# Kernel optimization log

Measured on AMD Instinct MI355X. Metric: run time of the kernel, lower is better.

## Reference

```python
import jax, jax.numpy as jnp
import numpy as np

D_STATE = 16
D_CONV = 4


def _diag_perm(H, W):
    perm = []
    for off in range(-(H - 1), W):
        for i in range(H):
            j = i + off
            if 0 <= j < W:
                perm.append(i * W + j)
    perm = np.asarray(perm, dtype=np.int32)
    inv = np.argsort(perm).astype(np.int32)
    return perm, inv


def _mamba_block(x, W_in, conv_w, W_xproj, W_dt, b_dt, A_log, W_outm):
    # x: [B, L, E]; shared-weight SimplifiedMambaBlock, expand=1 -> d_inner = E
    Bsz, L, E = x.shape
    d_inner = W_in.shape[1] // 2
    d_state = W_xproj.shape[1] // 2
    xz = x @ W_in                              # [B, L, 2*d_inner]
    xi, z = xz[..., :d_inner], xz[..., d_inner:]
    # causal depthwise conv1d (padding=d_conv-1, trimmed to L)
    xc = jax.lax.conv_general_dilated(
        xi.transpose(0, 2, 1), conv_w, window_strides=(1,),
        padding=[(conv_w.shape[-1] - 1, 0)], feature_group_count=d_inner,
        dimension_numbers=('NCH', 'OIH', 'NCH'))
    xc = jax.nn.silu(xc.transpose(0, 2, 1))    # [B, L, d_inner]
    dtbc = xc @ W_xproj                        # [B, L, 2*d_state]
    dt = jax.nn.softplus(dtbc[..., :d_state] @ W_dt + b_dt)  # [B, L, d_inner]
    Bc = dtbc[..., d_state:]                   # [B, L, d_state]
    A = -jnp.exp(A_log)                        # [d_inner, d_state]

    def step(h, inp):
        dt_t, B_t, x_t = inp                   # [B,d_inner], [B,d_state], [B,d_inner]
        h = h * jnp.exp(A[None] * dt_t[:, :, None]) + B_t[:, None, :] * x_t[:, :, None]
        return h, h.sum(-1)

    h0 = jnp.zeros((Bsz, d_inner, d_state), x.dtype)
    _, y = jax.lax.scan(step, h0, (dt.transpose(1, 0, 2), Bc.transpose(1, 0, 2), xc.transpose(1, 0, 2)))
    y = y.transpose(1, 0, 2)                   # [B, L, d_inner]
    return (y * jax.nn.silu(z)) @ W_outm


def setup_inputs() -> dict:
    key = jax.random.key(0)
    ks = jax.random.split(key, 16)
    B, H, W, E = 8, 32, 32, 1024
    d_inner, d_state = E, D_STATE
    s = lambda n: 1.0 / np.sqrt(n)
    A = np.tile(np.arange(1, d_state + 1, dtype=np.float32), (d_inner, 1))
    return {
        'vision_features': jax.random.normal(ks[0], (B, H * W, E), jnp.float32),
        'W_input': jax.random.normal(ks[1], (E, E), jnp.float32) * s(E),
        'W_in': jax.random.normal(ks[2], (E, 2 * d_inner), jnp.float32) * s(E),
        'conv_w': jax.random.normal(ks[3], (d_inner, 1, D_CONV), jnp.float32) * s(D_CONV),
        'W_xproj': jax.random.normal(ks[4], (d_inner, 2 * d_state), jnp.float32) * s(d_inner),
        'W_dt': jax.random.normal(ks[5], (d_state, d_inner), jnp.float32) * s(d_state),
        'b_dt': jax.random.normal(ks[6], (d_inner,), jnp.float32) * 0.01,
        'A_log': jnp.asarray(np.log(A)),
        'W_outm': jax.random.normal(ks[7], (d_inner, E), jnp.float32) * s(d_inner),
        'dir_w': jnp.full((4,), 0.25, jnp.float32),
        'ln_g': jnp.ones((E,), jnp.float32),
        'ln_b': jnp.zeros((E,), jnp.float32),
        'W_outproj': jax.random.normal(ks[8], (E, E), jnp.float32) * s(E),
        'Wg1': jax.random.normal(ks[9], (E, E // 4), jnp.float32) * s(E),
        'Wg2': jax.random.normal(ks[10], (E // 4, 1), jnp.float32) * s(E // 4),
        'height': H,
        'width': W,
    }


def reference(vision_features, W_input, W_in, conv_w, W_xproj, W_dt, b_dt, A_log,
              W_outm, dir_w, ln_g, ln_b, W_outproj, Wg1, Wg2, height, width):
    B, N, E = vision_features.shape
    H, Wd = int(height), int(width)
    mamba = lambda t: _mamba_block(t, W_in, conv_w, W_xproj, W_dt, b_dt, A_log, W_outm)
    x = vision_features @ W_input              # [B, N, E]
    x2d = x.reshape(B, H, Wd, E)
    # direction 1: row-major
    out1 = mamba(x)
    # direction 2: flipped both spatial dims
    xf = jnp.flip(x2d, (1, 2)).reshape(B, N, E)
    out2 = jnp.flip(mamba(xf).reshape(B, H, Wd, E), (1, 2)).reshape(B, N, E)
    # direction 3: column-major (transpose)
    xt = x2d.transpose(0, 2, 1, 3).reshape(B, N, E)
    out3 = mamba(xt).reshape(B, Wd, H, E).transpose(0, 2, 1, 3).reshape(B, N, E)
    # direction 4: anti-diagonal scan
    perm, inv = _diag_perm(H, Wd)
    out4 = mamba(x[:, perm])[:, inv]
    fused = dir_w[0] * out1 + dir_w[1] * out2 + dir_w[2] * out3 + dir_w[3] * out4
    mu = fused.mean(-1, keepdims=True)
    var = ((fused - mu) ** 2).mean(-1, keepdims=True)
    fused = (fused - mu) * jax.lax.rsqrt(var + 1e-5) * ln_g + ln_b
    enhanced = fused @ W_outproj
    g = jax.nn.sigmoid(jax.nn.silu(vision_features.mean(1, keepdims=True) @ Wg1) @ Wg2)  # [B,1,1]
    return vision_features + g * enhanced
```

## Files before the change

### kernel.cpp

```cpp
#include <hip/hip_runtime.h>

typedef unsigned short u16;
typedef unsigned int u32;
typedef short v8s __attribute__((ext_vector_type(8)));
typedef float v4f __attribute__((ext_vector_type(4)));
typedef float v2f __attribute__((ext_vector_type(2)));

#define B_SZ 8
#define HH 32
#define WW 32
#define NN 1024
#define M1 (B_SZ * NN)
#define M4 (4 * M1)
#define NCHUNK 32
#define CLEN 32
#define CTB 8

__device__ __forceinline__ float bf2f(u16 u) {
    u32 x = ((u32)u) << 16;
    return __builtin_bit_cast(float, x);
}
__device__ __forceinline__ u16 f2bf(float f) {
    u32 x = __builtin_bit_cast(u32, f);
    x = x + 0x7fffu + ((x >> 16) & 1u);
    return (u16)(x >> 16);
}
__device__ __forceinline__ float sigmoidf_(float x) { return 1.f / (1.f + __expf(-x)); }
__device__ __forceinline__ float ldf(const void* p, size_t i, int fin) {
    return fin ? ((const float*)p)[i] : bf2f(((const u16*)p)[i]);
}
__device__ __forceinline__ u16 ldbf(const void* p, size_t i, int fin) {
    return fin ? f2bf(((const float*)p)[i]) : ((const u16*)p)[i];
}
__device__ __forceinline__ void gload_lds16(const u16* g, u16* l) {
    __builtin_amdgcn_global_load_lds(
        (const __attribute__((address_space(1))) unsigned int*)g,
        (__attribute__((address_space(3))) unsigned int*)l, 16, 0, 0);
}
__device__ __forceinline__ int dirmap(int d, int t, const int* __restrict__ perm3) {
    if (d == 0) return t;
    if (d == 1) return (NN - 1) - t;
    if (d == 2) return (t & (HH - 1)) * WW + (t >> 5);
    return perm3[t];
}

__global__ void detect_dtype(const u16* __restrict__ raw, int* __restrict__ flags) {
    if (threadIdx.x == 0 && blockIdx.x == 0) {
        int ok = 0;
        for (int i = 0; i < 512; i++) {
            int e = (raw[i] >> 7) & 0xFF;
            ok += (e >= 100 && e <= 140) ? 1 : 0;
        }
        flags[0] = (ok < 460) ? 1 : 0;
    }
}

__global__ __launch_bounds__(256) void convert_bf(const void* __restrict__ src,
                                                  u16* __restrict__ dst,
                                                  const int* __restrict__ flags, int n) {
    int fin = flags[0];
    int i = blockIdx.x * 256 + threadIdx.x;
    if (i < n) dst[i] = ldbf(src, (size_t)i, fin);
}

__global__ __launch_bounds__(256) void zero_f32(float* __restrict__ p, int n) {
    int i = blockIdx.x * 256 + threadIdx.x;
    if (i < n) p[i] = 0.f;
}

__global__ void diag_perm_init(int* __restrict__ perm, int* __restrict__ inv) {
    int t = blockIdx.x * blockDim.x + threadIdx.x;
    if (t >= NN) return;
    int i = t / WW, j = t % WW;
    int off = j - i;
    int start = 0;
    for (int o = -(HH - 1); o < off; ++o) {
        int lo = (0 > -o) ? 0 : -o;
        int hi = (HH - 1 < WW - 1 - o) ? (HH - 1) : (WW - 1 - o);
        start += (hi - lo + 1);
    }
    int lo0 = (0 > -off) ? 0 : -off;
    int r = start + (i - lo0);
    perm[r] = t;
    inv[t] = r;
}

__global__ __launch_bounds__(256) void transpose_pad(const void* __restrict__ src,
                                                     u16* __restrict__ dst,
                                                     int K, int Nsrc,
                                                     const int* __restrict__ flags) {
    int fin = flags[0];
    __shared__ u16 tile[32][33];
    int k0 = blockIdx.x * 32, n0 = blockIdx.y * 32;
    int tx = threadIdx.x & 31, ty = threadIdx.x >> 5;
#pragma unroll
    for (int i = 0; i < 4; i++) {
        int k = k0 + ty + i * 8, n = n0 + tx;
        tile[ty + i * 8][tx] = (n < Nsrc) ? ldbf(src, (size_t)k * Nsrc + n, fin) : (u16)0;
    }
    __syncthreads();
#pragma unroll
    for (int i = 0; i < 4; i++) {
        int n = n0 + ty + i * 8, k = k0 + tx;
        dst[(size_t)n * K + k] = tile[tx][ty + i * 8];
    }
}

template <int EM>
__global__ __launch_bounds__(256) void gemm128(const u16* __restrict__ A,
                                               const u16* __restrict__ Bt,
                                               void* __restrict__ out0,
                                               void* __restrict__ out1,
                                               int M, int N, int K,
                                               const int* __restrict__ flags,
                                               const void* __restrict__ aux0,
                                               const float* __restrict__ aux1) {
    int fin = flags[0];
    __shared__ __align__(16) u16 As[128][32];
    __shared__ __align__(16) u16 Bs[128][32];
    int tid = threadIdx.x;
    int wave = tid >> 6, lane = tid & 63, quad = lane >> 4, l16 = lane & 15;
    int wm = wave >> 1, wn = wave & 1;
    int m0 = blockIdx.x * 128, n0 = blockIdx.y * 128;
    int r = tid >> 2, p = tid & 3;
    int sA = ((p ^ ((r >> 1) & 3))) * 8;

    const u16* rA0 = A + (size_t)(m0 + r) * K;
    const u16* rA1 = A + (size_t)(m0 + 64 + r) * K;
    const u16* rB0 = Bt + (size_t)(n0 + r) * K;
    const u16* rB1 = Bt + (size_t)(n0 + 64 + r) * K;

    v4f acc[4][4];
#pragma unroll
    for (int i = 0; i < 4; i++)
#pragma unroll
        for (int j = 0; j < 4; j++) acc[i][j] = (v4f){0.f, 0.f, 0.f, 0.f};

    int swf = ((l16 >> 1) & 3);
    for (int k0 = 0; k0 < K; k0 += 32) {
        gload_lds16(rA0 + k0 + sA, &As[r][p * 8]);
        gload_lds16(rA1 + k0 + sA, &As[64 + r][p * 8]);
        gload_lds16(rB0 + k0 + sA, &Bs[r][p * 8]);
        gload_lds16(rB1 + k0 + sA, &Bs[64 + r][p * 8]);
        __syncthreads();
        v8s af[4], bf[4];
#pragma unroll
        for (int i = 0; i < 4; i++)
            af[i] = *(const v8s*)&As[wm * 64 + i * 16 + l16][(quad ^ swf) * 8];
#pragma unroll
        for (int j = 0; j < 4; j++)
            bf[j] = *(const v8s*)&Bs[wn * 64 + j * 16 + l16][(quad ^ swf) * 8];
#pragma unroll
        for (int i = 0; i < 4; i++)
#pragma unroll
            for (int j = 0; j < 4; j++)
                acc[i][j] = __builtin_amdgcn_mfma_f32_16x16x32_bf16(af[i], bf[j],
                                                                    acc[i][j], 0, 0, 0);
        __syncthreads();
    }

#pragma unroll
    for (int i = 0; i < 4; i++) {
#pragma unroll
        for (int j = 0; j < 4; j++) {
#pragma unroll
            for (int rr = 0; rr < 4; rr++) {
                int row = m0 + wm * 64 + i * 16 + quad * 4 + rr;
                int col = n0 + wn * 64 + j * 16 + l16;
                float v = acc[i][j][rr];
                size_t oi = (size_t)row * N + col;
                if (EM == 0) {
                    ((u16*)out0)[oi] = f2bf(v);
                } else if (EM == 1) {
                    if (col < 1024) ((u16*)out0)[(size_t)row * 1024 + col] = f2bf(v);
                    else ((u16*)out1)[(size_t)row * 1024 + (col - 1024)] = f2bf(v);
                } else {
                    float g = aux1[row >> 10];
                    float res = ldf(aux0, oi, fin) + g * v;
                    if (fin) ((float*)out0)[oi] = res;
                    else ((u16*)out0)[oi] = f2bf(res);
                }
            }
        }
    }
}

__global__ __launch_bounds__(256) void gemm_dtbc_ks(const u16* __restrict__ A,
                                                    const u16* __restrict__ Bt,
                                                    float* __restrict__ out0,
                                                    int M, int N, int K) {
    __shared__ u16 As[64][32];
    __shared__ u16 Bs[64][32];
    int tid = threadIdx.x;
    int wave = tid >> 6, lane = tid & 63, quad = lane >> 4, l16 = lane & 15;
    int m0 = blockIdx.x * 64;
    int kbase = blockIdx.y * 128;
    int lr = tid >> 2, p = tid & 3;
    int sA = ((p ^ ((lr >> 1) & 3))) * 8;
    const u16* arow = A + (size_t)(m0 + lr) * K + kbase;
    const u16* brow = Bt + (size_t)lr * K + kbase;
    v4f acc[4];
#pragma unroll
    for (int j = 0; j < 4; j++) acc[j] = (v4f){0.f, 0.f, 0.f, 0.f};
    int swf = ((l16 >> 1) & 3);
    for (int k0 = 0; k0 < 128; k0 += 32) {
        uint4 av = *(const uint4*)(arow + k0 + sA);
        uint4 bv = *(const uint4*)(brow + k0 + sA);
        *(uint4*)&As[lr][p * 8] = av;
        *(uint4*)&Bs[lr][p * 8] = bv;
        __syncthreads();
        v8s af = *(const v8s*)&As[wave * 16 + l16][(quad ^ swf) * 8];
#pragma unroll
        for (int j = 0; j < 4; j++) {
            v8s bf = *(const v8s*)&Bs[j * 16 + l16][(quad ^ swf) * 8];
            acc[j] = __builtin_amdgcn_mfma_f32_16x16x32_bf16(af, bf, acc[j], 0, 0, 0);
        }
        __syncthreads();
    }
#pragma unroll
    for (int j = 0; j < 4; j++)
#pragma unroll
        for (int rr = 0; rr < 4; rr++) {
            int row = m0 + wave * 16 + quad * 4 + rr;
            int col = j * 16 + l16;
            atomicAdd(&out0[(size_t)row * N + col], acc[j][rr]);
        }
}

__global__ __launch_bounds__(256) void conv_tile(const u16* __restrict__ xi,
                                                 const void* __restrict__ cw,
                                                 u16* __restrict__ xc4,
                                                 const int* __restrict__ flags,
                                                 const int* __restrict__ perm3) {
    int fin = flags[0];
    int gblk = blockIdx.x;
    int d = gblk >> 10, blk = gblk & 1023;
    int b = blk >> 7, tc = blk & 127;
    int t0 = tc * CTB;
    __shared__ u16 rows[CTB + 3][1024];
    __shared__ int sp[CTB + 3];
    if (threadIdx.x < CTB + 3) {
        int tt = t0 - 3 + (int)threadIdx.x;
        sp[threadIdx.x] = (tt >= 0) ? dirmap(d, tt, perm3) : -1;
    }
    __syncthreads();
    for (int i = threadIdx.x; i < (CTB + 3) * 128; i += 256) {
        int r = i >> 7, off = (i & 127) * 8;
        int src = sp[r];
        uint4 v = make_uint4(0, 0, 0, 0);
        if (src >= 0)
            v = *(const uint4*)(xi + ((size_t)(b * 1024 + src)) * 1024 + off);
        *(uint4*)&rows[r][off] = v;
    }
    int e0 = threadIdx.x * 4;
    float w[4][4];
#pragma unroll
    for (int ee = 0; ee < 4; ee++)
#pragma unroll
        for (int k = 0; k < 4; k++)
            w[ee][k] = ldf(cw, (size_t)(e0 + ee) * 4 + k, fin);
    __syncthreads();
    u16* outp = xc4 + (size_t)d * M1 * 1024;
#pragma unroll
    for (int t = 0; t < CTB; t++) {
        float a[4] = {0.f, 0.f, 0.f, 0.f};
#pragma unroll
        for (int k = 0; k < 4; k++) {
            uint2 v = *(const uint2*)&rows[t + k][e0];
            const u16* vs = (const u16*)&v;
#pragma unroll
            for (int ee = 0; ee < 4; ee++)
                a[ee] += w[ee][k] * bf2f(vs[ee]);
        }
        u16 o[4];
#pragma unroll
        for (int ee = 0; ee < 4; ee++) o[ee] = f2bf(a[ee] * sigmoidf_(a[ee]));
        *(uint2*)(outp + ((size_t)(b * 1024 + t0 + t)) * 1024 + e0) = *(const uint2*)o;
    }
}

#define SCAN_TLOOP(FASTV)                                                      \
    for (int t = 0; t < CLEN; t++) {                                           \
        float xn = 0.f, zn = 0.f;                                              \
        if (t + 1 < CLEN) {                                                    \
            xn = bf2f(xcyz[ix + 1024]);                                        \
            if (PASS == 3) zn = bf2f(zb[zbase + (size_t)s_perm[t + 1] * 1024]);\
        }                                                                      \
        v2f xpv = {bd, 0.f};                                                   \
        _Pragma("unroll")                                                      \
        for (int p = 0; p < 8; p++)                                            \
            xpv += (*(const v2f*)&sdt[t][2 * p]) * wdt2[p];                    \
        float xp = xpv.x + xpv.y;                                              \
        float ex = __expf(xp);                                                 \
        float dtv = (xp > 15.f) ? xp : __logf(1.f + ex);                       \
        v2f acc2 = {0.f, 0.f};                                                 \
        if (FASTV) {                                                           \
            float E = __expf(-dtv);                                            \
            v2f Ev; Ev.x = E; Ev.y = E * E;                                    \
            v2f Estep; Estep.x = Ev.y; Estep.y = Ev.y;                         \
            _Pragma("unroll")                                                  \
            for (int p = 0; p < 8; p++) {                                      \
                v2f bc = *(const v2f*)&sdt[t][16 + 2 * p];                     \
                h2[p] = h2[p] * Ev + bc * xv;                                  \
                acc2 += h2[p];                                                 \
                Ev *= Estep;                                                   \
            }                                                                  \
        } else {                                                               \
            _Pragma("unroll")                                                  \
            for (int p = 0; p < 8; p++) {                                      \
                v2f es;                                                        \
                es.x = __expf(Ae2[p].x * dtv);                                 \
                es.y = __expf(Ae2[p].y * dtv);                                 \
                v2f bc = *(const v2f*)&sdt[t][16 + 2 * p];                     \
                h2[p] = h2[p] * es + bc * xv;                                  \
                acc2 += h2[p];                                                 \
            }                                                                  \
        }                                                                      \
        if (PASS == 1) ds += dtv;                                              \
        if (PASS == 3) {                                                       \
            float accv = acc2.x + acc2.y;                                      \
            xcyz[ix] = f2bf(accv * (zv * sigmoidf_(zv)) * wd);                 \
        }                                                                      \
        ix += 1024;                                                            \
        xv = xn;                                                               \
        zv = zn;                                                               \
    }

template <int PASS>
__global__ __launch_bounds__(256) void scan_chunk(const float* __restrict__ dtbc,
                                                  u16* __restrict__ xcyz,
                                                  const u16* __restrict__ zb,
                                                  const void* __restrict__ A_log,
                                                  const void* __restrict__ W_dt,
                                                  const void* __restrict__ b_dt,
                                                  const int* __restrict__ flags,
                                                  float* __restrict__ hend,
                                                  float* __restrict__ dtsum,
                                                  const void* __restrict__ dirw,
                                                  const int* __restrict__ perm3) {
    int fin = flags[0];
    int bid = blockIdx.x;
    int ec = bid & 3, c = (bid >> 2) & 31, b = (bid >> 7) & 7, d = bid >> 10;
    int e = ec * 256 + threadIdx.x;
    size_t row0 = (size_t)d * M1 + b * 1024 + c * CLEN;
    size_t cix  = (size_t)d * 256 + b * NCHUNK + c;
    __shared__ float sdt[CLEN][32];
    __shared__ int s_perm[CLEN];
    {
        const float* src = dtbc + row0 * 64;
        int t = threadIdx.x >> 3, f = threadIdx.x & 7;
        *(float4*)&sdt[t][f * 4] = *(const float4*)(src + (size_t)t * 64 + f * 4);
        if (PASS == 3 && threadIdx.x < CLEN)
            s_perm[threadIdx.x] = dirmap(d, c * CLEN + (int)threadIdx.x, perm3);
    }
    v2f Ae2[8], wdt2[8];
    bool fast = true;
#pragma unroll
    for (int p = 0; p < 8; p++) {
        float a0 = -__expf(ldf(A_log, (size_t)e * 16 + 2 * p, fin));
        float a1 = -__expf(ldf(A_log, (size_t)e * 16 + 2 * p + 1, fin));
        Ae2[p].x = a0;
        Ae2[p].y = a1;
        fast = fast && fabsf(a0 + (float)(2 * p + 1)) < 1e-3f * (2 * p + 1)
                    && fabsf(a1 + (float)(2 * p + 2)) < 1e-3f * (2 * p + 2);
    }
#pragma unroll
    for (int p = 0; p < 8; p++) {
        wdt2[p].x = ldf(W_dt, (size_t)(2 * p) * 1024 + e, fin);
        wdt2[p].y = ldf(W_dt, (size_t)(2 * p + 1) * 1024 + e, fin);
    }
    float bd = ldf(b_dt, e, fin);
    float wd = (PASS == 3) ? ldf(dirw, d, fin) : 0.f;
    v2f h2[8];
    if (PASS == 1) {
#pragma unroll
        for (int p = 0; p < 8; p++) h2[p] = (v2f){0.f, 0.f};
    } else {
#pragma unroll
        for (int p = 0; p < 8; p++) {
            h2[p].x = hend[(cix * 16 + 2 * p) * 1024 + e];
            h2[p].y = hend[(cix * 16 + 2 * p + 1) * 1024 + e];
        }
    }
    __syncthreads();
    float ds = 0.f;
    size_t ix = row0 * 1024 + e;
    size_t zbase = (size_t)b * 1024 * 1024 + e;
    float xv = bf2f(xcyz[ix]);
    float zv = (PASS == 3) ? bf2f(zb[zbase + (size_t)s_perm[0] * 1024]) : 0.f;
    if (fast) {
        SCAN_TLOOP(true)
    } else {
        SCAN_TLOOP(false)
    }
    if (PASS == 1) {
#pragma unroll
        for (int p = 0; p < 8; p++) {
            hend[(cix * 16 + 2 * p) * 1024 + e] = h2[p].x;
            hend[(cix * 16 + 2 * p + 1) * 1024 + e] = h2[p].y;
        }
        dtsum[cix * 1024 + e] = ds;
    }
}

__global__ __launch_bounds__(256) void scan_combine2(float* __restrict__ hend,
                                                     const float* __restrict__ dtsum,
                                                     const void* __restrict__ A_log,
                                                     const int* __restrict__ flags) {
    int fin = flags[0];
    int bid = blockIdx.x;
    int ec = bid & 3, s = (bid >> 2) & 15, b = (bid >> 6) & 7, d = bid >> 9;
    int e = ec * 256 + threadIdx.x;
    float Ae = -__expf(ldf(A_log, (size_t)e * 16 + s, fin));
    float H = 0.f;
    size_t base = (size_t)d * 256 + (size_t)b * NCHUNK;
    for (int c = 0; c < NCHUNK; c++) {
        size_t cix = base + c;
        float ds = dtsum[cix * 1024 + e];
        size_t idx = (cix * 16 + s) * 1024 + e;
        float loc = hend[idx];
        hend[idx] = H;
        H = loc + __expf(Ae * ds) * H;
    }
}

__global__ __launch_bounds__(256) void ln4_kernel(const u16* __restrict__ y4,
                                                  const void* __restrict__ ln_g,
                                                  const void* __restrict__ ln_b,
                                                  const int* __restrict__ flags,
                                                  const int* __restrict__ inv3,
                                                  u16* __restrict__ fn) {
    int fin = flags[0];
    int row = blockIdx.x;
    int b = row >> 10, q = row & 1023;
    int t1 = 1023 - q;
    int t2 = ((q & 31) << 5) | (q >> 5);
    int t3 = inv3[q];
    const u16* p0 = y4 + ((size_t)(b * 1024 + q)) * 1024;
    const u16* p1 = y4 + ((size_t)(M1 + b * 1024 + t1)) * 1024;
    const u16* p2 = y4 + ((size_t)(2 * M1 + b * 1024 + t2)) * 1024;
    const u16* p3 = y4 + ((size_t)(3 * M1 + b * 1024 + t3)) * 1024;
    int e0 = threadIdx.x * 4;
    uint2 a0 = *(const uint2*)(p0 + e0);
    uint2 a1 = *(const uint2*)(p1 + e0);
    uint2 a2 = *(const uint2*)(p2 + e0);
    uint2 a3 = *(const uint2*)(p3 + e0);
    const u16* s0 = (const u16*)&a0;
    const u16* s1 = (const u16*)&a1;
    const u16* s2 = (const u16*)&a2;
    const u16* s3 = (const u16*)&a3;
    float v[4];
    float sum = 0.f, sq = 0.f;
#pragma unroll
    for (int j = 0; j < 4; j++) {
        float f = bf2f(s0[j]) + bf2f(s1[j]) + bf2f(s2[j]) + bf2f(s3[j]);
        v[j] = f;
        sum += f;
        sq += f * f;
    }
    __shared__ float r1[256], r2[256];
    r1[threadIdx.x] = sum;
    r2[threadIdx.x] = sq;
    __syncthreads();
    for (int s = 128; s > 0; s >>= 1) {
        if (threadIdx.x < s) {
            r1[threadIdx.x] += r1[threadIdx.x + s];
            r2[threadIdx.x] += r2[threadIdx.x + s];
        }
        __syncthreads();
    }
    float mu = r1[0] * (1.f / 1024.f);
    float var = r2[0] * (1.f / 1024.f) - mu * mu;
    float rs = rsqrtf(var + 1e-5f);
    u16 o[4];
#pragma unroll
    for (int j = 0; j < 4; j++) {
        int e = e0 + j;
        o[j] = f2bf((v[j] - mu) * rs * ldf(ln_g, e, fin) + ldf(ln_b, e, fin));
    }
    *(uint2*)(fn + (size_t)row * 1024 + e0) = *(const uint2*)o;
}

__global__ __launch_bounds__(256) void gate_partial(const u16* __restrict__ vfb,
                                                    float* __restrict__ meanv) {
    int b = blockIdx.x >> 4, tc = blockIdx.x & 15;
    float s[4] = {0.f, 0.f, 0.f, 0.f};
    const u16* base = vfb + ((size_t)b * 1024 + tc * 64) * 1024;
    for (int t = 0; t < 64; t++) {
#pragma unroll
        for (int k = 0; k < 4; k++)
            s[k] += bf2f(base[(size_t)t * 1024 + threadIdx.x + k * 256]);
    }
#pragma unroll
    for (int k = 0; k < 4; k++)
        atomicAdd(&meanv[b * 1024 + threadIdx.x + k * 256], s[k]);
}

__global__ __launch_bounds__(256) void gate_mv(const float* __restrict__ meanv,
                                               const void* __restrict__ Wg1,
                                               const int* __restrict__ flags,
                                               float* __restrict__ gpart) {
    int fin = flags[0];
    int kc = blockIdx.x, j = threadIdx.x;
    __shared__ float mv[8][32];
    if (threadIdx.x < 8 * 32) {
        int b = threadIdx.x >> 5, kk = threadIdx.x & 31;
        mv[b][kk] = meanv[b * 1024 + kc * 32 + kk] * (1.f / 1024.f);
    }
    __syncthreads();
    float acc[8];
#pragma unroll
    for (int b = 0; b < 8; b++) acc[b] = 0.f;
    for (int kk = 0; kk < 32; kk++) {
        float w = ldf(Wg1, (size_t)(kc * 32 + kk) * 256 + j, fin);
#pragma unroll
        for (int b = 0; b < 8; b++) acc[b] += mv[b][kk] * w;
    }
#pragma unroll
    for (int b = 0; b < 8; b++) atomicAdd(&gpart[b * 256 + j], acc[b]);
}

__global__ __launch_bounds__(256) void gate_fin2(const float* __restrict__ gpart,
                                                 const void* __restrict__ Wg2,
                                                 const int* __restrict__ flags,
                                                 float* __restrict__ g) {
    int fin = flags[0];
    int b = blockIdx.x, j = threadIdx.x;
    __shared__ float red[256];
    float a = gpart[b * 256 + j];
    float si = a * sigmoidf_(a);
    red[j] = si * ldf(Wg2, j, fin);
    __syncthreads();
    for (int st = 128; st > 0; st >>= 1) {
        if (j < st) red[j] += red[j + st];
        __syncthreads();
    }
    if (j == 0) g[b] = sigmoidf_(red[0]);
}

extern "C" void kernel_launch(void* const* d_in, const int* in_sizes, int n_in,
                              void* d_out, int out_size, void* d_ws, size_t ws_size,
                              hipStream_t stream) {
    const void* vf_raw  = d_in[0];
    const void* W_input = d_in[1];
    const void* W_in    = d_in[2];
    const void* conv_w  = d_in[3];
    const void* W_xproj = d_in[4];
    const void* W_dt    = d_in[5];
    const void* b_dt    = d_in[6];
    const void* A_log   = d_in[7];
    const void* W_outm  = d_in[8];
    const void* dir_w   = d_in[9];
    const void* ln_g    = d_in[10];
    const void* ln_b    = d_in[11];
    const void* W_outpj = d_in[12];
    const void* Wg1     = d_in[13];
    const void* Wg2     = d_in[14];

    char* ws = (char*)d_ws;
    size_t off = 0;
    auto alloc = [&](size_t bytes) -> void* {
        void* p = ws + off;
        off = (off + bytes + 255) & ~(size_t)255;
        return p;
    };
    int*   flags = (int*)alloc(256);
    int*   perm3 = (int*)alloc(NN * 4);
    int*   inv3  = (int*)alloc(NN * 4);
    float* meanv = (float*)alloc(8 * 1024 * 4);
    float* gpart = (float*)alloc(8 * 256 * 4);
    float* gbuf  = (float*)alloc(64);
    u16*   WtI   = (u16*)alloc((size_t)1024 * 1024 * 2);
    u16*   WtIn  = (u16*)alloc((size_t)2048 * 1024 * 2);
    u16*   WtXp  = (u16*)alloc((size_t)64 * 1024 * 2);
    u16*   WtOm  = (u16*)alloc((size_t)1024 * 1024 * 2);
    u16*   WtOp  = (u16*)alloc((size_t)1024 * 1024 * 2);
    u16*   vfb   = (u16*)alloc((size_t)M1 * 1024 * 2);
    u16*   xbuf  = (u16*)alloc((size_t)M1 * 1024 * 2);
    float* tail32= (float*)alloc((size_t)M1 * 1024 * 4);
    u16*   xi    = (u16*)alloc((size_t)M1 * 1024 * 2);
    u16*   zb    = (u16*)alloc((size_t)M1 * 1024 * 2);
    u16*   xc4   = (u16*)alloc((size_t)M4 * 1024 * 2);
    float* dtbc4 = (float*)alloc((size_t)M4 * 64 * 4);
    float* dtsum4= (float*)alloc((size_t)4 * 8 * NCHUNK * 1024 * 4);
    float* hend4 = (float*)vfb;
    u16*   y4    = (u16*)vfb;
    (void)tail32;

    detect_dtype<<<1, 64, 0, stream>>>((const u16*)vf_raw, flags);
    convert_bf<<<(M1 * 1024) / 256, 256, 0, stream>>>(vf_raw, vfb, flags, M1 * 1024);
    diag_perm_init<<<4, 256, 0, stream>>>(perm3, inv3);
    transpose_pad<<<dim3(32, 32), 256, 0, stream>>>(W_input, WtI, 1024, 1024, flags);
    transpose_pad<<<dim3(32, 64), 256, 0, stream>>>(W_in, WtIn, 1024, 2048, flags);
    transpose_pad<<<dim3(32, 2), 256, 0, stream>>>(W_xproj, WtXp, 1024, 32, flags);
    transpose_pad<<<dim3(32, 32), 256, 0, stream>>>(W_outm, WtOm, 1024, 1024, flags);
    transpose_pad<<<dim3(32, 32), 256, 0, stream>>>(W_outpj, WtOp, 1024, 1024, flags);
    zero_f32<<<32, 256, 0, stream>>>(meanv, 8 * 1024);
    zero_f32<<<8, 256, 0, stream>>>(gpart, 8 * 256);

    gate_partial<<<128, 256, 0, stream>>>(vfb, meanv);
    gate_mv<<<32, 256, 0, stream>>>(meanv, Wg1, flags, gpart);
    gate_fin2<<<8, 256, 0, stream>>>(gpart, Wg2, flags, gbuf);

    gemm128<0><<<dim3(64, 8), 256, 0, stream>>>(
        vfb, WtI, xbuf, nullptr, M1, 1024, 1024, flags, nullptr, nullptr);
    gemm128<1><<<dim3(64, 16), 256, 0, stream>>>(
        xbuf, WtIn, xi, zb, M1, 2048, 1024, flags, nullptr, nullptr);

    conv_tile<<<4096, 256, 0, stream>>>(xi, conv_w, xc4, flags, perm3);
    zero_f32<<<(M4 * 64) / 256, 256, 0, stream>>>(dtbc4, M4 * 64);
    gemm_dtbc_ks<<<dim3(512, 8), 256, 0, stream>>>(xc4, WtXp, dtbc4, M4, 64, 1024);
    scan_chunk<1><<<4096, 256, 0, stream>>>(dtbc4, xc4, zb, A_log, W_dt, b_dt,
                                            flags, hend4, dtsum4, dir_w, perm3);
    scan_combine2<<<2048, 256, 0, stream>>>(hend4, dtsum4, A_log, flags);
    scan_chunk<3><<<4096, 256, 0, stream>>>(dtbc4, xc4, zb, A_log, W_dt, b_dt,
                                            flags, hend4, dtsum4, dir_w, perm3);

    gemm128<0><<<dim3(256, 8), 256, 0, stream>>>(
        xc4, WtOm, y4, nullptr, M4, 1024, 1024, flags, nullptr, nullptr);

    u16* fn = xi;
    ln4_kernel<<<M1, 256, 0, stream>>>(y4, ln_g, ln_b, flags, inv3, fn);
    gemm128<4><<<dim3(64, 8), 256, 0, stream>>>(
        fn, WtOp, d_out, nullptr, M1, 1024, 1024, flags, vf_raw, gbuf);
}
```

Baseline: 737.5 us.

## Narrow GEMM N-tile for small GEMMs and simplify softplus decay in scan

Templates the 128-row GEMM on a column-tile width so the smaller M1-row GEMMs use a 64-column tile and launch twice as many blocks, which should fill more compute units. In the scan's fast path (A = -(s+1)), the decay exp(-softplus(x)) is computed directly as 1/(1+e^x), dropping a log and an exp. The per-chunk dt sum is replaced by a running product of decays, and the combine kernel raises that product to the integer power s+1 by repeated squaring instead of calling exp. The product form can underflow across long chunks and changes rounding slightly. The combine kernel also reloads 16 A_log values per thread to decide whether the fast path applies.

```diff
diff --git a/kernel.cpp b/kernel.cpp
--- a/kernel.cpp
+++ b/kernel.cpp
@@ -106,7 +106,7 @@
     }
 }
 
-template <int EM>
+template <int EM, int WJ>
 __global__ __launch_bounds__(256) void gemm128(const u16* __restrict__ A,
                                                const u16* __restrict__ Bt,
                                                void* __restrict__ out0,
@@ -115,13 +115,14 @@
                                                const int* __restrict__ flags,
                                                const void* __restrict__ aux0,
                                                const float* __restrict__ aux1) {
+    constexpr int BN = WJ * 32;
     int fin = flags[0];
     __shared__ __align__(16) u16 As[128][32];
-    __shared__ __align__(16) u16 Bs[128][32];
+    __shared__ __align__(16) u16 Bs[BN][32];
     int tid = threadIdx.x;
     int wave = tid >> 6, lane = tid & 63, quad = lane >> 4, l16 = lane & 15;
     int wm = wave >> 1, wn = wave & 1;
-    int m0 = blockIdx.x * 128, n0 = blockIdx.y * 128;
+    int m0 = blockIdx.x * 128, n0 = blockIdx.y * BN;
     int r = tid >> 2, p = tid & 3;
     int sA = ((p ^ ((r >> 1) & 3))) * 8;
 
@@ -130,30 +131,31 @@
     const u16* rB0 = Bt + (size_t)(n0 + r) * K;
     const u16* rB1 = Bt + (size_t)(n0 + 64 + r) * K;
 
-    v4f acc[4][4];
+    v4f acc[4][WJ];
 #pragma unroll
     for (int i = 0; i < 4; i++)
 #pragma unroll
-        for (int j = 0; j < 4; j++) acc[i][j] = (v4f){0.f, 0.f, 0.f, 0.f};
+        for (int j = 0; j < WJ; j++) acc[i][j] = (v4f){0.f, 0.f, 0.f, 0.f};
 
     int swf = ((l16 >> 1) & 3);
     for (int k0 = 0; k0 < K; k0 += 32) {
         gload_lds16(rA0 + k0 + sA, &As[r][p * 8]);
         gload_lds16(rA1 + k0 + sA, &As[64 + r][p * 8]);
         gload_lds16(rB0 + k0 + sA, &Bs[r][p * 8]);
-        gload_lds16(rB1 + k0 + sA, &Bs[64 + r][p * 8]);
+        if constexpr (WJ == 4)
+            gload_lds16(rB1 + k0 + sA, &Bs[64 + r][p * 8]);
         __syncthreads();
-        v8s af[4], bf[4];
+        v8s af[4], bf[WJ];
 #pragma unroll
         for (int i = 0; i < 4; i++)
             af[i] = *(const v8s*)&As[wm * 64 + i * 16 + l16][(quad ^ swf) * 8];
 #pragma unroll
-        for (int j = 0; j < 4; j++)
-            bf[j] = *(const v8s*)&Bs[wn * 64 + j * 16 + l16][(quad ^ swf) * 8];
+        for (int j = 0; j < WJ; j++)
+            bf[j] = *(const v8s*)&Bs[wn * (WJ * 16) + j * 16 + l16][(quad ^ swf) * 8];
 #pragma unroll
         for (int i = 0; i < 4; i++)
 #pragma unroll
-            for (int j = 0; j < 4; j++)
+            for (int j = 0; j < WJ; j++)
                 acc[i][j] = __builtin_amdgcn_mfma_f32_16x16x32_bf16(af[i], bf[j],
                                                                     acc[i][j], 0, 0, 0);
         __syncthreads();
@@ -162,11 +164,11 @@
 #pragma unroll
     for (int i = 0; i < 4; i++) {
 #pragma unroll
-        for (int j = 0; j < 4; j++) {
+        for (int j = 0; j < WJ; j++) {
 #pragma unroll
             for (int rr = 0; rr < 4; rr++) {
                 int row = m0 + wm * 64 + i * 16 + quad * 4 + rr;
-                int col = n0 + wn * 64 + j * 16 + l16;
+                int col = n0 + wn * (WJ * 16) + j * 16 + l16;
                 float v = acc[i][j][rr];
                 size_t oi = (size_t)row * N + col;
                 if (EM == 0) {
@@ -292,10 +294,9 @@
             xpv += (*(const v2f*)&sdt[t][2 * p]) * wdt2[p];                    \
         float xp = xpv.x + xpv.y;                                              \
         float ex = __expf(xp);                                                 \
-        float dtv = (xp > 15.f) ? xp : __logf(1.f + ex);                       \
         v2f acc2 = {0.f, 0.f};                                                 \
         if (FASTV) {                                                           \
-            float E = __expf(-dtv);                                            \
+            float E = 1.f / (1.f + ex);        \
             v2f Ev; Ev.x = E; Ev.y = E * E;                                    \
             v2f Estep; Estep.x = Ev.y; Estep.y = Ev.y;                         \
             _Pragma("unroll")                                                  \
@@ -305,7 +306,9 @@
                 acc2 += h2[p];                                                 \
                 Ev *= Estep;                                                   \
             }                                                                  \
+            if (PASS == 1) ds *= E;                   \
         } else {                                                               \
+            float dtv = (xp > 15.f) ? xp : __logf(1.f + ex);                   \
             _Pragma("unroll")                                                  \
             for (int p = 0; p < 8; p++) {                                      \
                 v2f es;                                                        \
@@ -315,8 +318,8 @@
                 h2[p] = h2[p] * es + bc * xv;                                  \
                 acc2 += h2[p];                                                 \
             }                                                                  \
+            if (PASS == 1) ds += dtv;                                          \
         }                                                                      \
-        if (PASS == 1) ds += dtv;                                              \
         if (PASS == 3) {                                                       \
             float accv = acc2.x + acc2.y;                                      \
             xcyz[ix] = f2bf(accv * (zv * sigmoidf_(zv)) * wd);                 \
@@ -383,7 +386,7 @@
         }
     }
     __syncthreads();
-    float ds = 0.f;
+    float ds = fast ? 1.f : 0.f;
     size_t ix = row0 * 1024 + e;
     size_t zbase = (size_t)b * 1024 * 1024 + e;
     float xv = bf2f(xcyz[ix]);
@@ -411,16 +414,35 @@
     int bid = blockIdx.x;
     int ec = bid & 3, s = (bid >> 2) & 15, b = (bid >> 6) & 7, d = bid >> 9;
     int e = ec * 256 + threadIdx.x;
+    bool fast = true;
+#pragma unroll
+    for (int s2 = 0; s2 < 16; s2++) {
+        float a = -__expf(ldf(A_log, (size_t)e * 16 + s2, fin));
+        fast = fast && fabsf(a + (float)(s2 + 1)) < 1e-3f * (s2 + 1);
+    }
     float Ae = -__expf(ldf(A_log, (size_t)e * 16 + s, fin));
     float H = 0.f;
     size_t base = (size_t)d * 256 + (size_t)b * NCHUNK;
     for (int c = 0; c < NCHUNK; c++) {
         size_t cix = base + c;
         float ds = dtsum[cix * 1024 + e];
+        float decay;
+        if (fast) {
+            float r = 1.f, bb = ds;
+            int n = s + 1;
+            while (n) {
+                if (n & 1) r *= bb;
+                bb *= bb;
+                n >>= 1;
+            }
+            decay = r;
+        } else {
+            decay = __expf(Ae * ds);
+        }
         size_t idx = (cix * 16 + s) * 1024 + e;
         float loc = hend[idx];
         hend[idx] = H;
-        H = loc + __expf(Ae * ds) * H;
+        H = loc + decay * H;
     }
 }
 
@@ -602,9 +624,9 @@
     gate_mv<<<32, 256, 0, stream>>>(meanv, Wg1, flags, gpart);
     gate_fin2<<<8, 256, 0, stream>>>(gpart, Wg2, flags, gbuf);
 
-    gemm128<0><<<dim3(64, 8), 256, 0, stream>>>(
+    gemm128<0, 2><<<dim3(64, 16), 256, 0, stream>>>(
         vfb, WtI, xbuf, nullptr, M1, 1024, 1024, flags, nullptr, nullptr);
-    gemm128<1><<<dim3(64, 16), 256, 0, stream>>>(
+    gemm128<1, 2><<<dim3(64, 32), 256, 0, stream>>>(
         xbuf, WtIn, xi, zb, M1, 2048, 1024, flags, nullptr, nullptr);
 
     conv_tile<<<4096, 256, 0, stream>>>(xi, conv_w, xc4, flags, perm3);
@@ -616,11 +638,11 @@
     scan_chunk<3><<<4096, 256, 0, stream>>>(dtbc4, xc4, zb, A_log, W_dt, b_dt,
                                             flags, hend4, dtsum4, dir_w, perm3);
 
-    gemm128<0><<<dim3(256, 8), 256, 0, stream>>>(
+    gemm128<0, 4><<<dim3(256, 8), 256, 0, stream>>>(
         xc4, WtOm, y4, nullptr, M4, 1024, 1024, flags, nullptr, nullptr);
 
     u16* fn = xi;
     ln4_kernel<<<M1, 256, 0, stream>>>(y4, ln_g, ln_b, flags, inv3, fn);
-    gemm128<4><<<dim3(64, 8), 256, 0, stream>>>(
+    gemm128<4, 2><<<dim3(64, 16), 256, 0, stream>>>(
         fn, WtOp, d_out, nullptr, M1, 1024, 1024, flags, vf_raw, gbuf);
 }
```

After: 755.4 us. +2.4%, slower.
